# Performance work log

Measured on AMD Instinct MI355X. Metric: run time of the kernel, lower is better.

Reference implementation:

```python
import jax, jax.numpy as jnp
import numpy as np

B, S, C, H = 256, 512, 512, 512
MOG_ITERS = 5


def _xavier(key, shape):
    fan_out, fan_in = shape
    lim = float(np.sqrt(6.0 / (fan_in + fan_out)))
    return jax.random.uniform(key, shape, minval=-lim, maxval=lim, dtype=jnp.float32)


def setup_inputs() -> dict:
    key = jax.random.key(0)
    ks = jax.random.split(key, 7)
    x = jax.random.normal(ks[0], (B, S, C), dtype=jnp.float32)
    return {
        "x": x,
        "Wih_w": _xavier(ks[1], (4 * H, C)), "Wih_b": jnp.zeros((4 * H,), jnp.float32),
        "Wmx_w": _xavier(ks[2], (H, C)),     "Wmx_b": jnp.zeros((H,), jnp.float32),
        "Wmh_w": _xavier(ks[3], (H, H)),     "Wmh_b": jnp.zeros((H,), jnp.float32),
        "Whm_w": _xavier(ks[4], (4 * H, H)), "Whm_b": jnp.zeros((4 * H,), jnp.float32),
        "Q": _xavier(ks[5], (H, C)),
        "R": _xavier(ks[6], (C, H)),
    }


def _mogrify(xt, ht, Q, R):
    # alternating mogrifier rounds; odd i updates xt, even i updates ht
    for i in range(1, MOG_ITERS + 1):
        if i % 2 == 1:
            xt = 2.0 * jax.nn.sigmoid(ht @ Q) * xt  # (B,H)@(H,C) -> (B,C)
        else:
            ht = 2.0 * jax.nn.sigmoid(xt @ R) * ht  # (B,C)@(C,H) -> (B,H)
    return xt, ht


def reference(x, Wih_w, Wih_b, Wmx_w, Wmx_b, Wmh_w, Wmh_b, Whm_w, Whm_b, Q, R):
    batch = x.shape[0]
    h0 = jnp.zeros((batch, H), x.dtype)
    c0 = jnp.zeros((batch, H), x.dtype)

    def step(carry, xt):
        ht, Ct = carry
        xt, ht = _mogrify(xt, ht, Q, R)
        mt = xt @ Wmx_w.T + Wmx_b + ht @ Wmh_w.T + Wmh_b          # (B,H)
        gates = xt @ Wih_w.T + Wih_b + mt @ Whm_w.T + Whm_b        # (B,4H)
        i_g, f_g, g_g, o_g = jnp.split(gates, 4, axis=1)
        Ct = jax.nn.sigmoid(f_g) * Ct + jax.nn.sigmoid(i_g) * jnp.tanh(g_g)
        ht = jax.nn.sigmoid(o_g) * jnp.tanh(Ct)
        return (ht, Ct), ht

    xs = jnp.swapaxes(x, 0, 1)                  # (S,B,C)
    _, hs = jax.lax.scan(step, (h0, c0), xs)    # (S,B,H)
    return jnp.swapaxes(hs, 0, 1)               # (B,S,H)
```

## Files before the change

kernel.cpp:

```cpp
#include <hip/hip_runtime.h>
#include <hip/hip_bf16.h>

#define Bdim 256
#define Sdim 512
#define Cdim 512
#define Hdim 512

typedef __attribute__((ext_vector_type(8))) short bfrag;
typedef __attribute__((ext_vector_type(8))) unsigned short u16x8;
typedef __attribute__((ext_vector_type(4))) float f32x4;

__device__ __forceinline__ unsigned short f2bf_rne(float f) {
    union { float f; unsigned u; } v; v.f = f;
    return (unsigned short)((v.u + 0x7fffu + ((v.u >> 16) & 1u)) >> 16);
}
__device__ __forceinline__ float sigmoidf_(float x) { return 1.0f / (1.0f + __expf(-x)); }

template<bool TRANS>
__global__ __launch_bounds__(256) void pack_weight(const float* __restrict__ src,
                                                   unsigned short* __restrict__ dst,
                                                   int K, int N) {
    int tid = blockIdx.x * 256 + threadIdx.x;
    int total = (K >> 5) * (N >> 4) * 64;
    if (tid >= total) return;
    int lane = tid & 63;
    int blk  = tid >> 6;
    int kc   = blk & 15;
    int n16  = blk >> 4;
    int n  = (n16 << 4) + (lane & 15);
    int kb = (kc << 5) + ((lane >> 4) << 3);
    u16x8 v;
#pragma unroll
    for (int j = 0; j < 8; ++j) {
        int k = kb + j;
        float f = TRANS ? src[(size_t)n * K + k] : src[(size_t)k * N + n];
        v[j] = f2bf_rne(f);
    }
    *(u16x8*)(dst + ((size_t)tid << 3)) = v;
}

__global__ __launch_bounds__(256) void zero_state(float* hf, float* cs, unsigned short* hb) {
    int tid = blockIdx.x * 256 + threadIdx.x;
    if (tid < Bdim * Hdim) { hf[tid] = 0.f; cs[tid] = 0.f; hb[tid] = 0; }
}

__global__ __launch_bounds__(64)
void mog_kernel(const unsigned short* __restrict__ A,
                const unsigned short* __restrict__ Wp,
                const float* __restrict__ prev, long prevStride,
                float* __restrict__ dstf, unsigned short* __restrict__ dstb)
{
    int nt = blockIdx.x, mt = blockIdx.y;
    int lane = threadIdx.x, lm = lane & 15, lq = lane >> 4;
    f32x4 acc[2][2] = {};
    const bfrag* A0 = (const bfrag*)(A + (size_t)(mt*32 +      lm) * 512) + lq;
    const bfrag* A1 = (const bfrag*)(A + (size_t)(mt*32 + 16 + lm) * 512) + lq;
    const bfrag* B0 = (const bfrag*)(Wp + (size_t)(nt*2    ) * 16 * 512) + lane;
    const bfrag* B1 = (const bfrag*)(Wp + (size_t)(nt*2 + 1) * 16 * 512) + lane;
#pragma unroll 4
    for (int kc = 0; kc < 16; ++kc) {
        bfrag a0 = A0[kc*4], a1 = A1[kc*4];
        bfrag b0 = B0[kc*64], b1 = B1[kc*64];
        acc[0][0] = __builtin_amdgcn_mfma_f32_16x16x32_bf16(a0, b0, acc[0][0], 0, 0, 0);
        acc[0][1] = __builtin_amdgcn_mfma_f32_16x16x32_bf16(a0, b1, acc[0][1], 0, 0, 0);
        acc[1][0] = __builtin_amdgcn_mfma_f32_16x16x32_bf16(a1, b0, acc[1][0], 0, 0, 0);
        acc[1][1] = __builtin_amdgcn_mfma_f32_16x16x32_bf16(a1, b1, acc[1][1], 0, 0, 0);
    }
    int nb = nt*32, mb = mt*32;
#pragma unroll
    for (int mi = 0; mi < 2; ++mi)
#pragma unroll
    for (int ni = 0; ni < 2; ++ni) {
        int n = nb + ni*16 + lm;
#pragma unroll
        for (int r = 0; r < 4; ++r) {
            int m = mb + mi*16 + lq*4 + r;
            float g = 2.0f * sigmoidf_(acc[mi][ni][r]);
            float v = g * prev[(size_t)m * prevStride + n];
            dstf[(size_t)m * 512 + n] = v;
            dstb[(size_t)m * 512 + n] = f2bf_rne(v);
        }
    }
}

__global__ __launch_bounds__(64)
void mt_kernel(const unsigned short* __restrict__ X,
               const unsigned short* __restrict__ Hm,
               const unsigned short* __restrict__ W1p,
               const unsigned short* __restrict__ W2p,
               const float* __restrict__ b1, const float* __restrict__ b2,
               unsigned short* __restrict__ mtb)
{
    int nt = blockIdx.x, mt = blockIdx.y;
    int lane = threadIdx.x, lm = lane & 15, lq = lane >> 4;
    f32x4 acc[2][2] = {};
    const unsigned short* As[2] = {X, Hm};
    const unsigned short* Ws[2] = {W1p, W2p};
#pragma unroll
    for (int ph = 0; ph < 2; ++ph) {
        const bfrag* A0 = (const bfrag*)(As[ph] + (size_t)(mt*32 +      lm) * 512) + lq;
        const bfrag* A1 = (const bfrag*)(As[ph] + (size_t)(mt*32 + 16 + lm) * 512) + lq;
        const bfrag* B0 = (const bfrag*)(Ws[ph] + (size_t)(nt*2    ) * 16 * 512) + lane;
        const bfrag* B1 = (const bfrag*)(Ws[ph] + (size_t)(nt*2 + 1) * 16 * 512) + lane;
#pragma unroll 4
        for (int kc = 0; kc < 16; ++kc) {
            bfrag a0 = A0[kc*4], a1 = A1[kc*4];
            bfrag b0 = B0[kc*64], b1 = B1[kc*64];
            acc[0][0] = __builtin_amdgcn_mfma_f32_16x16x32_bf16(a0, b0, acc[0][0], 0, 0, 0);
            acc[0][1] = __builtin_amdgcn_mfma_f32_16x16x32_bf16(a0, b1, acc[0][1], 0, 0, 0);
            acc[1][0] = __builtin_amdgcn_mfma_f32_16x16x32_bf16(a1, b0, acc[1][0], 0, 0, 0);
            acc[1][1] = __builtin_amdgcn_mfma_f32_16x16x32_bf16(a1, b1, acc[1][1], 0, 0, 0);
        }
    }
    int nb = nt*32, mb = mt*32;
#pragma unroll
    for (int mi = 0; mi < 2; ++mi)
#pragma unroll
    for (int ni = 0; ni < 2; ++ni) {
        int n = nb + ni*16 + lm;
        float bias = b1[n] + b2[n];
#pragma unroll
        for (int r = 0; r < 4; ++r) {
            int m = mb + mi*16 + lq*4 + r;
            mtb[(size_t)m * 512 + n] = f2bf_rne(acc[mi][ni][r] + bias);
        }
    }
}

__global__ __launch_bounds__(64)
void gates_cell_kernel(const unsigned short* __restrict__ X,
                       const unsigned short* __restrict__ Mt,
                       const unsigned short* __restrict__ Wihp,
                       const unsigned short* __restrict__ Whmp,
                       const float* __restrict__ bih, const float* __restrict__ bhm,
                       float* __restrict__ Cs, float* __restrict__ hf,
                       unsigned short* __restrict__ hb,
                       float* __restrict__ outp )
{
    int nt = blockIdx.x, mt = blockIdx.y;
    int lane = threadIdx.x, lm = lane & 15, lq = lane >> 4;
    f32x4 acc[4][2][2] = {};
    const unsigned short* As[2] = {X, Mt};
    const unsigned short* Ws[2] = {Wihp, Whmp};
#pragma unroll
    for (int ph = 0; ph < 2; ++ph) {
        const bfrag* A0 = (const bfrag*)(As[ph] + (size_t)(mt*32 +      lm) * 512) + lq;
        const bfrag* A1 = (const bfrag*)(As[ph] + (size_t)(mt*32 + 16 + lm) * 512) + lq;
        const unsigned short* W = Ws[ph];
#pragma unroll 2
        for (int kc = 0; kc < 16; ++kc) {
            bfrag a0 = A0[kc*4], a1 = A1[kc*4];
#pragma unroll
            for (int g = 0; g < 4; ++g) {
                const bfrag* B0 = (const bfrag*)(W + ((size_t)(g*32 + nt*2) * 16 + kc) * 512) + lane;
                bfrag b0 = B0[0];
                bfrag b1 = B0[1024];
                acc[g][0][0] = __builtin_amdgcn_mfma_f32_16x16x32_bf16(a0, b0, acc[g][0][0], 0, 0, 0);
                acc[g][0][1] = __builtin_amdgcn_mfma_f32_16x16x32_bf16(a0, b1, acc[g][0][1], 0, 0, 0);
                acc[g][1][0] = __builtin_amdgcn_mfma_f32_16x16x32_bf16(a1, b0, acc[g][1][0], 0, 0, 0);
                acc[g][1][1] = __builtin_amdgcn_mfma_f32_16x16x32_bf16(a1, b1, acc[g][1][1], 0, 0, 0);
            }
        }
    }
    int nb = nt*32, mb = mt*32;
#pragma unroll
    for (int mi = 0; mi < 2; ++mi)
#pragma unroll
    for (int ni = 0; ni < 2; ++ni) {
        int n = nb + ni*16 + lm;
        float bi = bih[n]        + bhm[n];
        float bf = bih[512 + n]  + bhm[512 + n];
        float bg = bih[1024 + n] + bhm[1024 + n];
        float bo = bih[1536 + n] + bhm[1536 + n];
#pragma unroll
        for (int r = 0; r < 4; ++r) {
            int m = mb + mi*16 + lq*4 + r;
            size_t idx = (size_t)m * 512 + n;
            float ig = sigmoidf_(acc[0][mi][ni][r] + bi);
            float fg = sigmoidf_(acc[1][mi][ni][r] + bf);
            float gg = tanhf    (acc[2][mi][ni][r] + bg);
            float og = sigmoidf_(acc[3][mi][ni][r] + bo);
            float c  = fg * Cs[idx] + ig * gg;
            Cs[idx] = c;
            float h = og * tanhf(c);
            hf[idx] = h;
            hb[idx] = f2bf_rne(h);
            outp[(size_t)m * (Sdim * Hdim) + n] = h;
        }
    }
}

extern "C" void kernel_launch(void* const* d_in, const int* in_sizes, int n_in,
                              void* d_out, int out_size, void* d_ws, size_t ws_size,
                              hipStream_t stream) {
    const float* x     = (const float*)d_in[0];
    const float* Wih_w = (const float*)d_in[1];
    const float* Wih_b = (const float*)d_in[2];
    const float* Wmx_w = (const float*)d_in[3];
    const float* Wmx_b = (const float*)d_in[4];
    const float* Wmh_w = (const float*)d_in[5];
    const float* Wmh_b = (const float*)d_in[6];
    const float* Whm_w = (const float*)d_in[7];
    const float* Whm_b = (const float*)d_in[8];
    const float* Q     = (const float*)d_in[9];
    const float* R     = (const float*)d_in[10];
    float* out = (float*)d_out;

    unsigned short* packQ   = (unsigned short*)d_ws;
    unsigned short* packR   = packQ   + 512 * 512;
    unsigned short* packWmx = packR   + 512 * 512;
    unsigned short* packWmh = packWmx + 512 * 512;
    unsigned short* packWih = packWmh + 512 * 512;
    unsigned short* packWhm = packWih + 512 * 2048;
    float* xtf = (float*)(packWhm + 512 * 2048);
    float* hf  = xtf + Bdim * Cdim;
    float* cs  = hf  + Bdim * Hdim;
    unsigned short* xtb = (unsigned short*)(cs + Bdim * Hdim);
    unsigned short* hb  = xtb + Bdim * Cdim;
    unsigned short* mtb = hb  + Bdim * Hdim;

    pack_weight<false><<<dim3(128), dim3(256), 0, stream>>>(Q,     packQ,   512, 512);
    pack_weight<false><<<dim3(128), dim3(256), 0, stream>>>(R,     packR,   512, 512);
    pack_weight<true ><<<dim3(128), dim3(256), 0, stream>>>(Wmx_w, packWmx, 512, 512);
    pack_weight<true ><<<dim3(128), dim3(256), 0, stream>>>(Wmh_w, packWmh, 512, 512);
    pack_weight<true ><<<dim3(512), dim3(256), 0, stream>>>(Wih_w, packWih, 512, 2048);
    pack_weight<true ><<<dim3(512), dim3(256), 0, stream>>>(Whm_w, packWhm, 512, 2048);
    zero_state<<<dim3(512), dim3(256), 0, stream>>>(hf, cs, hb);

    dim3 grid(16, 8), block(64);
    for (int t = 0; t < Sdim; ++t) {
        const float* xsrc = x + (size_t)t * Cdim;
        mog_kernel<<<grid, block, 0, stream>>>(hb,  packQ, xsrc, (long)(Sdim * Cdim), xtf, xtb);
        mog_kernel<<<grid, block, 0, stream>>>(xtb, packR, hf,   512, hf,  hb);
        mog_kernel<<<grid, block, 0, stream>>>(hb,  packQ, xtf,  512, xtf, xtb);
        mog_kernel<<<grid, block, 0, stream>>>(xtb, packR, hf,   512, hf,  hb);
        mog_kernel<<<grid, block, 0, stream>>>(hb,  packQ, xtf,  512, xtf, xtb);
        mt_kernel<<<grid, block, 0, stream>>>(xtb, hb, packWmx, packWmh, Wmx_b, Wmh_b, mtb);
        gates_cell_kernel<<<grid, block, 0, stream>>>(xtb, mtb, packWih, packWhm,
                                                      Wih_b, Whm_b, cs, hf, hb,
                                                      out + (size_t)t * Hdim);
    }
}
```

Baseline: 34.99 ms.

## Fold mt projection into gate weights and run persistent flag-synchronized kernel

Precomputes effective gate weights (Wih + Whm·Wmx and Whm·Wmh) and a folded bias, which removes the mt GEMM. The 3584 per-timestep launches are replaced by a single persistent kernel of 256 single-wave blocks: 16 batch partitions of 16 rows, each split into 16 column slices. Slices within a partition synchronise through agent-scope atomic flags, and state is kept in registers and a packed bf16 fragment layout. This targets launch overhead and inter-kernel gaps, at the cost of spin-wait synchronisation, a reliance on all blocks being co-resident, and a changed rounding order from folding the weights.

Result: faster. 30.93 ms (-11.6%).

```diff
diff --git a/kernel.cpp b/kernel.cpp
--- a/kernel.cpp
+++ b/kernel.cpp
@@ -1,10 +1,11 @@
 #include <hip/hip_runtime.h>
-#include <hip/hip_bf16.h>
 
 #define Bdim 256
 #define Sdim 512
 #define Cdim 512
 #define Hdim 512
+#define NP 16
+#define NSLICE 16
 
 typedef __attribute__((ext_vector_type(8))) short bfrag;
 typedef __attribute__((ext_vector_type(8))) unsigned short u16x8;
@@ -39,154 +40,197 @@
     *(u16x8*)(dst + ((size_t)tid << 3)) = v;
 }
 
-__global__ __launch_bounds__(256) void zero_state(float* hf, float* cs, unsigned short* hb) {
+__global__ __launch_bounds__(256) void weff_kernel(const float* __restrict__ A,
+                                                   const float* __restrict__ Whm,
+                                                   const float* __restrict__ Wadd,
+                                                   float* __restrict__ C) {
+    int n = blockIdx.x;
+    int k = blockIdx.y * 256 + threadIdx.x;
+    const float* wrow = Whm + (size_t)n * 512;
+    float acc = 0.f;
+#pragma unroll 8
+    for (int j = 0; j < 512; ++j) acc += A[(size_t)j * 512 + k] * wrow[j];
+    if (Wadd) acc += Wadd[(size_t)n * 512 + k];
+    C[(size_t)k * 2048 + n] = acc;
+}
+
+__global__ __launch_bounds__(256) void beff_kernel(const float* __restrict__ bmx,
+                                                   const float* __restrict__ bmh,
+                                                   const float* __restrict__ Whm,
+                                                   const float* __restrict__ bih,
+                                                   const float* __restrict__ bhm,
+                                                   float* __restrict__ beff) {
+    int n = blockIdx.x * 256 + threadIdx.x;
+    const float* wrow = Whm + (size_t)n * 512;
+    float acc = bih[n] + bhm[n];
+#pragma unroll 8
+    for (int j = 0; j < 512; ++j) acc += (bmx[j] + bmh[j]) * wrow[j];
+    beff[n] = acc;
+}
+
+__global__ __launch_bounds__(256) void init_state(unsigned short* __restrict__ Hg,
+                                                  unsigned short* __restrict__ Hm,
+                                                  int* __restrict__ flags) {
     int tid = blockIdx.x * 256 + threadIdx.x;
-    if (tid < Bdim * Hdim) { hf[tid] = 0.f; cs[tid] = 0.f; hb[tid] = 0; }
+    if (tid < NP * NSLICE) flags[tid] = 0;
+    for (int i = tid; i < NP * 8192; i += gridDim.x * 256) { Hg[i] = 0; Hm[i] = 0; }
+}
+
+
+__device__ __forceinline__ bfrag afrag_load(const unsigned short* F, int kc, int lane) {
+    union { unsigned long long u[2]; bfrag f; } v;
+    const unsigned long long* pp = (const unsigned long long*)(F + kc * 512 + lane * 8);
+    v.u[0] = __hip_atomic_load(pp,     __ATOMIC_RELAXED, __HIP_MEMORY_SCOPE_AGENT);
+    v.u[1] = __hip_atomic_load(pp + 1, __ATOMIC_RELAXED, __HIP_MEMORY_SCOPE_AGENT);
+    return v.f;
+}
+
+__device__ __forceinline__ void store_pair(unsigned short* Dst, int m, int n,
+                                           unsigned short b, int lane) {
+    unsigned pb = __shfl_xor((unsigned)b, 1);
+    if (!(lane & 1)) {
+        unsigned word = (unsigned)b | (pb << 16);
+        int idx = ((n >> 5) << 9) + (((m & 15) + ((n >> 3) & 3) * 16) << 3) + (n & 7);
+        __hip_atomic_store((unsigned*)(Dst + idx), word,
+                           __ATOMIC_RELAXED, __HIP_MEMORY_SCOPE_AGENT);
+    }
+}
+
+__device__ __forceinline__ void wait_flags(const int* fl, int target, int lane) {
+    while (true) {
+        int f = __hip_atomic_load(fl + (lane & 15), __ATOMIC_RELAXED, __HIP_MEMORY_SCOPE_AGENT);
+        if (__all(f >= target)) break;
+        __builtin_amdgcn_s_sleep(1);
+    }
+    asm volatile("" ::: "memory");
+}
+
+__device__ __forceinline__ void post_flag(int* fl, int s, int qnew, int lane) {
+    asm volatile("s_waitcnt vmcnt(0)" ::: "memory");
+    if (lane == 0)
+        __hip_atomic_store(fl + s, qnew, __ATOMIC_RELAXED, __HIP_MEMORY_SCOPE_AGENT);
+}
+
+__device__ __forceinline__ void mog_stage(const unsigned short* __restrict__ Af,
+                                          const unsigned short* __restrict__ Wp,
+                                          unsigned short* __restrict__ Dst,
+                                          float pv[2][4],
+                                          int s, int lane, int lm, int lq) {
+    f32x4 acc[2] = {};
+    const bfrag* B = (const bfrag*)Wp + (size_t)s * 2048 + lane;
+#pragma unroll 8
+    for (int kc = 0; kc < 16; ++kc) {
+        bfrag a = afrag_load(Af, kc, lane);
+        acc[0] = __builtin_amdgcn_mfma_f32_16x16x32_bf16(a, B[kc * 64],        acc[0], 0, 0, 0);
+        acc[1] = __builtin_amdgcn_mfma_f32_16x16x32_bf16(a, B[1024 + kc * 64], acc[1], 0, 0, 0);
+    }
+#pragma unroll
+    for (int nt = 0; nt < 2; ++nt)
+#pragma unroll
+        for (int r = 0; r < 4; ++r) {
+            int n = s * 32 + nt * 16 + lm;
+            int m = lq * 4 + r;
+            float v = 2.0f * sigmoidf_(acc[nt][r]) * pv[nt][r];
+            pv[nt][r] = v;
+            store_pair(Dst, m, n, f2bf_rne(v), lane);
+        }
 }
 
 __global__ __launch_bounds__(64)
-void mog_kernel(const unsigned short* __restrict__ A,
-                const unsigned short* __restrict__ Wp,
-                const float* __restrict__ prev, long prevStride,
-                float* __restrict__ dstf, unsigned short* __restrict__ dstb)
-{
-    int nt = blockIdx.x, mt = blockIdx.y;
-    int lane = threadIdx.x, lm = lane & 15, lq = lane >> 4;
-    f32x4 acc[2][2] = {};
-    const bfrag* A0 = (const bfrag*)(A + (size_t)(mt*32 +      lm) * 512) + lq;
-    const bfrag* A1 = (const bfrag*)(A + (size_t)(mt*32 + 16 + lm) * 512) + lq;
-    const bfrag* B0 = (const bfrag*)(Wp + (size_t)(nt*2    ) * 16 * 512) + lane;
-    const bfrag* B1 = (const bfrag*)(Wp + (size_t)(nt*2 + 1) * 16 * 512) + lane;
+void moglstm_persistent(const float* __restrict__ x,
+                        const unsigned short* __restrict__ Qp,
+                        const unsigned short* __restrict__ Rp,
+                        const unsigned short* __restrict__ WXp,
+                        const unsigned short* __restrict__ WHp,
+                        const float* __restrict__ beff,
+                        unsigned short* __restrict__ Xb,
+                        unsigned short* __restrict__ Hmb,
+                        unsigned short* __restrict__ Hgb,
+                        int* __restrict__ flags,
+                        float* __restrict__ out) {
+    const int w = blockIdx.x;
+    const int p = w >> 4, s = w & 15;
+    const int lane = threadIdx.x & 63, lm = lane & 15, lq = lane >> 4;
+    unsigned short* Xp = Xb + p * 8192;
+    unsigned short* Hm = Hmb + p * 8192;
+    unsigned short* Hg = Hgb + p * 8192;
+    int* fl = flags + p * NSLICE;
+
+    float px[2][4];
+    float ph[2][4] = {};
+    float cst[2][4] = {};
+    float bia[4][2];
+#pragma unroll
+    for (int g = 0; g < 4; ++g)
+#pragma unroll
+        for (int nt = 0; nt < 2; ++nt)
+            bia[g][nt] = beff[g * 512 + s * 32 + nt * 16 + lm];
+
+    const size_t xbase = (size_t)(p * 16) * Sdim * Cdim;
+    const size_t obase = (size_t)(p * 16) * Sdim * Hdim;
+
+    int q = 0;
+#pragma unroll 1
+    for (int t = 0; t < Sdim; ++t) {
+#pragma unroll
+        for (int nt = 0; nt < 2; ++nt)
+#pragma unroll
+            for (int r = 0; r < 4; ++r) {
+                int n = s * 32 + nt * 16 + lm;
+                int m = lq * 4 + r;
+                px[nt][r] = x[xbase + (size_t)m * (Sdim * Cdim) + (size_t)t * Cdim + n];
+            }
+        wait_flags(fl, q, lane);
+        mog_stage(Hg, Qp, Xp, px, s, lane, lm, lq);
+        post_flag(fl, s, ++q, lane);
+        wait_flags(fl, q, lane);
+        mog_stage(Xp, Rp, Hm, ph, s, lane, lm, lq);
+        post_flag(fl, s, ++q, lane);
+        wait_flags(fl, q, lane);
+        mog_stage(Hm, Qp, Xp, px, s, lane, lm, lq);
+        post_flag(fl, s, ++q, lane);
+        wait_flags(fl, q, lane);
+        mog_stage(Xp, Rp, Hm, ph, s, lane, lm, lq);
+        post_flag(fl, s, ++q, lane);
+        wait_flags(fl, q, lane);
+        mog_stage(Hm, Qp, Xp, px, s, lane, lm, lq);
+        post_flag(fl, s, ++q, lane);
+        wait_flags(fl, q, lane);
+        {
+            f32x4 acc[4][2] = {};
 #pragma unroll 4
-    for (int kc = 0; kc < 16; ++kc) {
-        bfrag a0 = A0[kc*4], a1 = A1[kc*4];
-        bfrag b0 = B0[kc*64], b1 = B1[kc*64];
-        acc[0][0] = __builtin_amdgcn_mfma_f32_16x16x32_bf16(a0, b0, acc[0][0], 0, 0, 0);
-        acc[0][1] = __builtin_amdgcn_mfma_f32_16x16x32_bf16(a0, b1, acc[0][1], 0, 0, 0);
-        acc[1][0] = __builtin_amdgcn_mfma_f32_16x16x32_bf16(a1, b0, acc[1][0], 0, 0, 0);
-        acc[1][1] = __builtin_amdgcn_mfma_f32_16x16x32_bf16(a1, b1, acc[1][1], 0, 0, 0);
-    }
-    int nb = nt*32, mb = mt*32;
-#pragma unroll
-    for (int mi = 0; mi < 2; ++mi)
-#pragma unroll
-    for (int ni = 0; ni < 2; ++ni) {
-        int n = nb + ni*16 + lm;
-#pragma unroll
-        for (int r = 0; r < 4; ++r) {
-            int m = mb + mi*16 + lq*4 + r;
-            float g = 2.0f * sigmoidf_(acc[mi][ni][r]);
-            float v = g * prev[(size_t)m * prevStride + n];
-            dstf[(size_t)m * 512 + n] = v;
-            dstb[(size_t)m * 512 + n] = f2bf_rne(v);
+            for (int kc = 0; kc < 16; ++kc) {
+                bfrag aX = afrag_load(Xp, kc, lane);
+                bfrag aH = afrag_load(Hm, kc, lane);
+#pragma unroll
+                for (int g = 0; g < 4; ++g) {
+                    const bfrag* BX = (const bfrag*)WXp + (size_t)((g * 32 + s * 2) * 16 + kc) * 64 + lane;
+                    const bfrag* BH = (const bfrag*)WHp + (size_t)((g * 32 + s * 2) * 16 + kc) * 64 + lane;
+                    acc[g][0] = __builtin_amdgcn_mfma_f32_16x16x32_bf16(aX, BX[0],    acc[g][0], 0, 0, 0);
+                    acc[g][0] = __builtin_amdgcn_mfma_f32_16x16x32_bf16(aH, BH[0],    acc[g][0], 0, 0, 0);
+                    acc[g][1] = __builtin_amdgcn_mfma_f32_16x16x32_bf16(aX, BX[1024], acc[g][1], 0, 0, 0);
+                    acc[g][1] = __builtin_amdgcn_mfma_f32_16x16x32_bf16(aH, BH[1024], acc[g][1], 0, 0, 0);
+                }
+            }
+#pragma unroll
+            for (int nt = 0; nt < 2; ++nt)
+#pragma unroll
+                for (int r = 0; r < 4; ++r) {
+                    int n = s * 32 + nt * 16 + lm;
+                    int m = lq * 4 + r;
+                    float ig = sigmoidf_(acc[0][nt][r] + bia[0][nt]);
+                    float fg = sigmoidf_(acc[1][nt][r] + bia[1][nt]);
+                    float gg = tanhf(acc[2][nt][r] + bia[2][nt]);
+                    float og = sigmoidf_(acc[3][nt][r] + bia[3][nt]);
+                    float c = fg * cst[nt][r] + ig * gg;
+                    cst[nt][r] = c;
+                    float h = og * tanhf(c);
+                    ph[nt][r] = h;
+                    store_pair(Hg, m, n, f2bf_rne(h), lane);
+                    out[obase + (size_t)m * (Sdim * Hdim) + (size_t)t * Hdim + n] = h;
+                }
         }
-    }
-}
-
-__global__ __launch_bounds__(64)
-void mt_kernel(const unsigned short* __restrict__ X,
-               const unsigned short* __restrict__ Hm,
-               const unsigned short* __restrict__ W1p,
-               const unsigned short* __restrict__ W2p,
-               const float* __restrict__ b1, const float* __restrict__ b2,
-               unsigned short* __restrict__ mtb)
-{
-    int nt = blockIdx.x, mt = blockIdx.y;
-    int lane = threadIdx.x, lm = lane & 15, lq = lane >> 4;
-    f32x4 acc[2][2] = {};
-    const unsigned short* As[2] = {X, Hm};
-    const unsigned short* Ws[2] = {W1p, W2p};
-#pragma unroll
-    for (int ph = 0; ph < 2; ++ph) {
-        const bfrag* A0 = (const bfrag*)(As[ph] + (size_t)(mt*32 +      lm) * 512) + lq;
-        const bfrag* A1 = (const bfrag*)(As[ph] + (size_t)(mt*32 + 16 + lm) * 512) + lq;
-        const bfrag* B0 = (const bfrag*)(Ws[ph] + (size_t)(nt*2    ) * 16 * 512) + lane;
-        const bfrag* B1 = (const bfrag*)(Ws[ph] + (size_t)(nt*2 + 1) * 16 * 512) + lane;
-#pragma unroll 4
-        for (int kc = 0; kc < 16; ++kc) {
-            bfrag a0 = A0[kc*4], a1 = A1[kc*4];
-            bfrag b0 = B0[kc*64], b1 = B1[kc*64];
-            acc[0][0] = __builtin_amdgcn_mfma_f32_16x16x32_bf16(a0, b0, acc[0][0], 0, 0, 0);
-            acc[0][1] = __builtin_amdgcn_mfma_f32_16x16x32_bf16(a0, b1, acc[0][1], 0, 0, 0);
-            acc[1][0] = __builtin_amdgcn_mfma_f32_16x16x32_bf16(a1, b0, acc[1][0], 0, 0, 0);
-            acc[1][1] = __builtin_amdgcn_mfma_f32_16x16x32_bf16(a1, b1, acc[1][1], 0, 0, 0);
-        }
-    }
-    int nb = nt*32, mb = mt*32;
-#pragma unroll
-    for (int mi = 0; mi < 2; ++mi)
-#pragma unroll
-    for (int ni = 0; ni < 2; ++ni) {
-        int n = nb + ni*16 + lm;
-        float bias = b1[n] + b2[n];
-#pragma unroll
-        for (int r = 0; r < 4; ++r) {
-            int m = mb + mi*16 + lq*4 + r;
-            mtb[(size_t)m * 512 + n] = f2bf_rne(acc[mi][ni][r] + bias);
-        }
-    }
-}
-
-__global__ __launch_bounds__(64)
-void gates_cell_kernel(const unsigned short* __restrict__ X,
-                       const unsigned short* __restrict__ Mt,
-                       const unsigned short* __restrict__ Wihp,
-                       const unsigned short* __restrict__ Whmp,
-                       const float* __restrict__ bih, const float* __restrict__ bhm,
-                       float* __restrict__ Cs, float* __restrict__ hf,
-                       unsigned short* __restrict__ hb,
-                       float* __restrict__ outp )
-{
-    int nt = blockIdx.x, mt = blockIdx.y;
-    int lane = threadIdx.x, lm = lane & 15, lq = lane >> 4;
-    f32x4 acc[4][2][2] = {};
-    const unsigned short* As[2] = {X, Mt};
-    const unsigned short* Ws[2] = {Wihp, Whmp};
-#pragma unroll
-    for (int ph = 0; ph < 2; ++ph) {
-        const bfrag* A0 = (const bfrag*)(As[ph] + (size_t)(mt*32 +      lm) * 512) + lq;
-        const bfrag* A1 = (const bfrag*)(As[ph] + (size_t)(mt*32 + 16 + lm) * 512) + lq;
-        const unsigned short* W = Ws[ph];
-#pragma unroll 2
-        for (int kc = 0; kc < 16; ++kc) {
-            bfrag a0 = A0[kc*4], a1 = A1[kc*4];
-#pragma unroll
-            for (int g = 0; g < 4; ++g) {
-                const bfrag* B0 = (const bfrag*)(W + ((size_t)(g*32 + nt*2) * 16 + kc) * 512) + lane;
-                bfrag b0 = B0[0];
-                bfrag b1 = B0[1024];
-                acc[g][0][0] = __builtin_amdgcn_mfma_f32_16x16x32_bf16(a0, b0, acc[g][0][0], 0, 0, 0);
-                acc[g][0][1] = __builtin_amdgcn_mfma_f32_16x16x32_bf16(a0, b1, acc[g][0][1], 0, 0, 0);
-                acc[g][1][0] = __builtin_amdgcn_mfma_f32_16x16x32_bf16(a1, b0, acc[g][1][0], 0, 0, 0);
-                acc[g][1][1] = __builtin_amdgcn_mfma_f32_16x16x32_bf16(a1, b1, acc[g][1][1], 0, 0, 0);
-            }
-        }
-    }
-    int nb = nt*32, mb = mt*32;
-#pragma unroll
-    for (int mi = 0; mi < 2; ++mi)
-#pragma unroll
-    for (int ni = 0; ni < 2; ++ni) {
-        int n = nb + ni*16 + lm;
-        float bi = bih[n]        + bhm[n];
-        float bf = bih[512 + n]  + bhm[512 + n];
-        float bg = bih[1024 + n] + bhm[1024 + n];
-        float bo = bih[1536 + n] + bhm[1536 + n];
-#pragma unroll
-        for (int r = 0; r < 4; ++r) {
-            int m = mb + mi*16 + lq*4 + r;
-            size_t idx = (size_t)m * 512 + n;
-            float ig = sigmoidf_(acc[0][mi][ni][r] + bi);
-            float fg = sigmoidf_(acc[1][mi][ni][r] + bf);
-            float gg = tanhf    (acc[2][mi][ni][r] + bg);
-            float og = sigmoidf_(acc[3][mi][ni][r] + bo);
-            float c  = fg * Cs[idx] + ig * gg;
-            Cs[idx] = c;
-            float h = og * tanhf(c);
-            hf[idx] = h;
-            hb[idx] = f2bf_rne(h);
-            outp[(size_t)m * (Sdim * Hdim) + n] = h;
-        }
+        post_flag(fl, s, ++q, lane);
     }
 }
 
@@ -206,38 +250,26 @@
     const float* R     = (const float*)d_in[10];
     float* out = (float*)d_out;
 
-    unsigned short* packQ   = (unsigned short*)d_ws;
-    unsigned short* packR   = packQ   + 512 * 512;
-    unsigned short* packWmx = packR   + 512 * 512;
-    unsigned short* packWmh = packWmx + 512 * 512;
-    unsigned short* packWih = packWmh + 512 * 512;
-    unsigned short* packWhm = packWih + 512 * 2048;
-    float* xtf = (float*)(packWhm + 512 * 2048);
-    float* hf  = xtf + Bdim * Cdim;
-    float* cs  = hf  + Bdim * Hdim;
-    unsigned short* xtb = (unsigned short*)(cs + Bdim * Hdim);
-    unsigned short* hb  = xtb + Bdim * Cdim;
-    unsigned short* mtb = hb  + Bdim * Hdim;
-
-    pack_weight<false><<<dim3(128), dim3(256), 0, stream>>>(Q,     packQ,   512, 512);
-    pack_weight<false><<<dim3(128), dim3(256), 0, stream>>>(R,     packR,   512, 512);
-    pack_weight<true ><<<dim3(128), dim3(256), 0, stream>>>(Wmx_w, packWmx, 512, 512);
-    pack_weight<true ><<<dim3(128), dim3(256), 0, stream>>>(Wmh_w, packWmh, 512, 512);
-    pack_weight<true ><<<dim3(512), dim3(256), 0, stream>>>(Wih_w, packWih, 512, 2048);
-    pack_weight<true ><<<dim3(512), dim3(256), 0, stream>>>(Whm_w, packWhm, 512, 2048);
-    zero_state<<<dim3(512), dim3(256), 0, stream>>>(hf, cs, hb);
-
-    dim3 grid(16, 8), block(64);
-    for (int t = 0; t < Sdim; ++t) {
-        const float* xsrc = x + (size_t)t * Cdim;
-        mog_kernel<<<grid, block, 0, stream>>>(hb,  packQ, xsrc, (long)(Sdim * Cdim), xtf, xtb);
-        mog_kernel<<<grid, block, 0, stream>>>(xtb, packR, hf,   512, hf,  hb);
-        mog_kernel<<<grid, block, 0, stream>>>(hb,  packQ, xtf,  512, xtf, xtb);
-        mog_kernel<<<grid, block, 0, stream>>>(xtb, packR, hf,   512, hf,  hb);
-        mog_kernel<<<grid, block, 0, stream>>>(hb,  packQ, xtf,  512, xtf, xtb);
-        mt_kernel<<<grid, block, 0, stream>>>(xtb, hb, packWmx, packWmh, Wmx_b, Wmh_b, mtb);
-        gates_cell_kernel<<<grid, block, 0, stream>>>(xtb, mtb, packWih, packWhm,
-                                                      Wih_b, Whm_b, cs, hf, hb,
-                                                      out + (size_t)t * Hdim);
-    }
-}
+    unsigned short* packQ  = (unsigned short*)d_ws;
+    unsigned short* packR  = packQ  + 512 * 512;
+    unsigned short* packWX = packR  + 512 * 512;
+    unsigned short* packWH = packWX + 512 * 2048;
+    unsigned short* Xb  = packWH + 512 * 2048;
+    unsigned short* Hmb = Xb  + NP * 8192;
+    unsigned short* Hgb = Hmb + NP * 8192;
+    float* beff    = (float*)(Hgb + NP * 8192);
+    float* scratch = beff + 2048;
+    int* flags     = (int*)(scratch + 512 * 2048);
+
+    pack_weight<false><<<dim3(128), dim3(256), 0, stream>>>(Q, packQ, 512, 512);
+    pack_weight<false><<<dim3(128), dim3(256), 0, stream>>>(R, packR, 512, 512);
+    weff_kernel<<<dim3(2048, 2), dim3(256), 0, stream>>>(Wmx_w, Whm_w, Wih_w, scratch);
+    pack_weight<false><<<dim3(512), dim3(256), 0, stream>>>(scratch, packWX, 512, 2048);
+    weff_kernel<<<dim3(2048, 2), dim3(256), 0, stream>>>(Wmh_w, Whm_w, nullptr, scratch);
+    pack_weight<false><<<dim3(512), dim3(256), 0, stream>>>(scratch, packWH, 512, 2048);
+    beff_kernel<<<dim3(8), dim3(256), 0, stream>>>(Wmx_b, Wmh_b, Whm_w, Wih_b, Whm_b, beff);
+    init_state<<<dim3(128), dim3(256), 0, stream>>>(Hgb, Hmb, flags);
+
+    moglstm_persistent<<<dim3(NP * NSLICE), dim3(64), 0, stream>>>(
+        x, packQ, packR, packWX, packWH, beff, Xb, Hmb, Hgb, flags, out);
+}
```
